# Performance work log

Hardware: AMD Instinct MI355X
Metric: run time of the kernel (lower is better)

The kernel has to match this reference:

```python
import jax, jax.numpy as jnp
import numpy as np

B, S, D = 4, 1024, 2048
NH, HD = 16, 128  # nhead, head_dim
SCALE = HD ** -0.5


def setup_inputs() -> dict:
    key = jax.random.key(0)
    ks = jax.random.split(key, 7)
    query = jax.random.normal(ks[0], (B, S, D), dtype=jnp.float32)
    key_t = jax.random.normal(ks[1], (B, S, D), dtype=jnp.float32)
    value = jax.random.normal(ks[2], (B, S, D), dtype=jnp.float32)
    # qkv_proj: Linear(D, 3D) with bias; out_proj: Linear(D, D) with bias
    Wqkv = jax.random.normal(ks[3], (3 * D, D), dtype=jnp.float32) * (D ** -0.5)
    bqkv = jnp.zeros((3 * D,), dtype=jnp.float32)
    Wout = jax.random.normal(ks[4], (D, D), dtype=jnp.float32) * (D ** -0.5)
    bout = jnp.zeros((D,), dtype=jnp.float32)
    return {"query": query, "key": key_t, "value": value,
            "Wqkv": Wqkv, "bqkv": bqkv, "Wout": Wout, "bout": bout}


def reference(query, key, value, Wqkv, bqkv, Wout, bout):
    # NOTE: module ignores `key`/`value` args; qkv comes from query alone.
    b, s, d = query.shape
    qkv = query @ Wqkv.T + bqkv                       # (B,S,3D)
    q, k, v = jnp.split(qkv, 3, axis=-1)
    q = q.reshape(b, s, NH, HD).transpose(0, 2, 1, 3) * SCALE  # (B,H,S,hd)
    k = k.reshape(b, s, NH, HD).transpose(0, 2, 1, 3)          # (B,H,S,hd)
    # faithful replication of the module's odd v permutation:
    v = v.reshape(b, s, HD, NH).transpose(0, 2, 1, 3)          # (B,hd,S,H)
    v = v.reshape(b, s, NH * HD).reshape(b, s, NH, HD).transpose(0, 2, 1, 3)  # (B,H,S,hd)
    scores = jnp.einsum('bhqd,bhkd->bhqk', q, k)               # (B,H,S,S)
    causal = jnp.triu(jnp.ones((s, s), dtype=bool), k=1)
    scores = jnp.where(causal, -jnp.inf, scores)
    attn = jax.nn.softmax(scores.astype(jnp.float32), axis=-1).astype(query.dtype)
    out = jnp.einsum('bhqk,bhkd->bhqd', attn, v)               # (B,H,S,hd)
    out = out.transpose(0, 2, 1, 3).reshape(b, s, d)
    return out @ Wout.T + bout
```

## Files before the change

kernel.cpp:

```cpp
#include <hip/hip_runtime.h>
#include <hip/hip_bf16.h>
#include <stdint.h>

typedef __bf16 bf16x8 __attribute__((ext_vector_type(8)));
typedef float  floatx4 __attribute__((ext_vector_type(4)));

#define NEG_BIG (-1e30f)

#define GLD16(g, l) __builtin_amdgcn_global_load_lds(                         \
    (__attribute__((address_space(1))) void*)(g),                             \
    (__attribute__((address_space(3))) void*)(l), 16, 0, 0)

__device__ __forceinline__ void cvt16(const float* __restrict__ s,
                                      __hip_bfloat16* __restrict__ d) {
    float4 f[4];
#pragma unroll
    for (int i = 0; i < 4; i++) f[i] = ((const float4*)s)[i];
    union { __hip_bfloat16 h[16]; uint4 u[2]; } o;
#pragma unroll
    for (int i = 0; i < 4; i++) {
        o.h[4 * i + 0] = __float2bfloat16(f[i].x);
        o.h[4 * i + 1] = __float2bfloat16(f[i].y);
        o.h[4 * i + 2] = __float2bfloat16(f[i].z);
        o.h[4 * i + 3] = __float2bfloat16(f[i].w);
    }
    ((uint4*)d)[0] = o.u[0];
    ((uint4*)d)[1] = o.u[1];
}

__global__ __launch_bounds__(256)
void cvt3_f32_bf16(const float* __restrict__ a, size_t na8,
                   const float* __restrict__ b, size_t nb8,
                   const float* __restrict__ c, size_t nc8,
                   __hip_bfloat16* __restrict__ da,
                   __hip_bfloat16* __restrict__ db,
                   __hip_bfloat16* __restrict__ dc)
{
    const size_t total  = na8 + nb8 + nc8;
    const size_t stride = (size_t)gridDim.x * blockDim.x;
    for (size_t idx = (size_t)blockIdx.x * blockDim.x + threadIdx.x;
         idx < total; idx += stride) {
        const float* s; __hip_bfloat16* d; size_t o;
        if (idx < na8)            { s = a; d = da; o = idx; }
        else if (idx < na8 + nb8) { s = b; d = db; o = idx - na8; }
        else                      { s = c; d = dc; o = idx - na8 - nb8; }
        const float4 f0 = ((const float4*)s)[o * 2 + 0];
        const float4 f1 = ((const float4*)s)[o * 2 + 1];
        union { __hip_bfloat16 h[8]; uint4 u; } z;
        z.h[0] = __float2bfloat16(f0.x); z.h[1] = __float2bfloat16(f0.y);
        z.h[2] = __float2bfloat16(f0.z); z.h[3] = __float2bfloat16(f0.w);
        z.h[4] = __float2bfloat16(f1.x); z.h[5] = __float2bfloat16(f1.y);
        z.h[6] = __float2bfloat16(f1.z); z.h[7] = __float2bfloat16(f1.w);
        ((uint4*)d)[o] = z.u;
    }
}

__global__ __launch_bounds__(256, 2)
void gemm2b_nt_bias(const __hip_bfloat16* __restrict__ A,
                    const __hip_bfloat16* __restrict__ B,
                    const float* __restrict__ bias,
                    __hip_bfloat16* __restrict__ C,
                    int M, int N, int K, int lda, int ldb)
{
    __shared__ __align__(16) __hip_bfloat16 Asm[2][128 * 64];
    __shared__ __align__(16) __hip_bfloat16 Bsm[2][192 * 64];

    const int flat = blockIdx.x;
    const int c    = flat & 7;
    const int i_   = flat >> 3;
    const int by = (c & 1) * 16 + (i_ & 15);
    const int bx = (c >> 1) * 8 + (i_ >> 4);
    const int m0 = by * 128, n0 = bx * 192;

    const int t    = threadIdx.x;
    const int wave = t >> 6, lane = t & 63;
    const int quad = lane >> 4, l16 = lane & 15;
    const int wr   = wave >> 1, wc = wave & 1;
    const int NT   = K >> 6;

    const int l8 = lane >> 3;
    const int g_ = (lane & 7) ^ l8;
    auto stageA = [&](int tk, int j, int buf) {
        GLD16(A + (size_t)(m0 + j * 32 + wave * 8 + l8) * lda + tk * 64 + g_ * 8,
              &Asm[buf][0] + (j * 32 + wave * 8) * 64);
    };
    auto stageB = [&](int tk, int j, int buf) {
        GLD16(B + (size_t)(n0 + j * 32 + wave * 8 + l8) * ldb + tk * 64 + g_ * 8,
              &Bsm[buf][0] + (j * 32 + wave * 8) * 64);
    };

    const int g0 = (quad ^ (l16 & 7)) << 3;

    floatx4 acc[4][6];
    const floatx4 zero = {0.f, 0.f, 0.f, 0.f};
#pragma unroll
    for (int mi = 0; mi < 4; mi++)
#pragma unroll
        for (int ni = 0; ni < 6; ni++) acc[mi][ni] = zero;

#pragma unroll
    for (int j = 0; j < 4; j++) stageA(0, j, 0);
#pragma unroll
    for (int j = 0; j < 6; j++) stageB(0, j, 0);
    if (NT > 1) {
        stageA(1, 0, 1); stageA(1, 2, 1);
        stageB(1, 0, 1); stageB(1, 1, 1); stageB(1, 2, 1);
        asm volatile("s_waitcnt vmcnt(5)" ::: "memory");
    } else {
        asm volatile("s_waitcnt vmcnt(0)" ::: "memory");
    }
    __syncthreads();

    int cb = 0;
    for (int tk = 0; tk < NT; ++tk, cb ^= 1) {
        const __hip_bfloat16* Ab = &Asm[cb][0];
        const __hip_bfloat16* Bb = &Bsm[cb][0];
        const int nb = cb ^ 1;

        bf16x8 af[2][2], bfr[6][2];
#pragma unroll
        for (int i = 0; i < 2; i++)
#pragma unroll
            for (int ks = 0; ks < 2; ks++)
                af[i][ks] = *(const bf16x8*)(
                    Ab + (wr * 64 + i * 16 + l16) * 64 + (g0 ^ (ks ? 32 : 0)));
#pragma unroll
        for (int ni = 0; ni < 6; ni++)
#pragma unroll
            for (int ks = 0; ks < 2; ks++)
                bfr[ni][ks] = *(const bf16x8*)(
                    Bb + (wc * 96 + ni * 16 + l16) * 64 + (g0 ^ (ks ? 32 : 0)));
        if (tk + 1 < NT) {
            stageA(tk + 1, 1, nb); stageA(tk + 1, 3, nb);
            stageB(tk + 1, 3, nb); stageB(tk + 1, 4, nb); stageB(tk + 1, 5, nb);
        }
        __builtin_amdgcn_s_barrier();
        asm volatile("s_waitcnt lgkmcnt(0)" ::: "memory");
        __builtin_amdgcn_s_setprio(1);
#pragma unroll
        for (int ks = 0; ks < 2; ks++)
#pragma unroll
            for (int i = 0; i < 2; i++)
#pragma unroll
                for (int ni = 0; ni < 6; ni++)
                    acc[i][ni] = __builtin_amdgcn_mfma_f32_16x16x32_bf16(
                        af[i][ks], bfr[ni][ks], acc[i][ni], 0, 0, 0);
        __builtin_amdgcn_s_setprio(0);
        __builtin_amdgcn_s_barrier();

#pragma unroll
        for (int i = 0; i < 2; i++)
#pragma unroll
            for (int ks = 0; ks < 2; ks++)
                af[i][ks] = *(const bf16x8*)(
                    Ab + (wr * 64 + (2 + i) * 16 + l16) * 64 + (g0 ^ (ks ? 32 : 0)));
        if (tk + 2 < NT) {
            stageA(tk + 2, 0, cb); stageA(tk + 2, 2, cb);
            stageB(tk + 2, 0, cb); stageB(tk + 2, 1, cb); stageB(tk + 2, 2, cb);
        }
        __builtin_amdgcn_s_barrier();
        asm volatile("s_waitcnt lgkmcnt(0)" ::: "memory");
        __builtin_amdgcn_s_setprio(1);
#pragma unroll
        for (int ks = 0; ks < 2; ks++)
#pragma unroll
            for (int i = 0; i < 2; i++)
#pragma unroll
                for (int ni = 0; ni < 6; ni++)
                    acc[2 + i][ni] = __builtin_amdgcn_mfma_f32_16x16x32_bf16(
                        af[i][ks], bfr[ni][ks], acc[2 + i][ni], 0, 0, 0);
        __builtin_amdgcn_s_setprio(0);
        if (tk + 2 < NT)
            asm volatile("s_waitcnt vmcnt(5)" ::: "memory");
        else if (tk + 1 < NT)
            asm volatile("s_waitcnt vmcnt(0)" ::: "memory");
        __builtin_amdgcn_s_barrier();
    }

#pragma unroll
    for (int mi = 0; mi < 4; mi++) {
        const int row = m0 + wr * 64 + mi * 16 + quad * 4;
#pragma unroll
        for (int ni = 0; ni < 6; ni++) {
            const int col = n0 + wc * 96 + ni * 16 + l16;
            const float bv = bias[col];
#pragma unroll
            for (int r = 0; r < 4; r++)
                C[(size_t)(row + r) * N + col] =
                    __float2bfloat16(acc[mi][ni][r] + bv);
        }
    }
}

template <bool OUT_F32>
__global__ __launch_bounds__(512, 2)
void gemm8p_nt_bias(const __hip_bfloat16* __restrict__ A,
                    const __hip_bfloat16* __restrict__ B,
                    const float* __restrict__ bias, void* __restrict__ Cv,
                    int M, int N, int K, int lda, int ldb, int nby)
{
    __shared__ __align__(16) __hip_bfloat16 Asm[2][128 * 64];
    __shared__ __align__(16) __hip_bfloat16 Bsm[2][256 * 64];

    const int nwg = gridDim.x, cpx = nwg >> 3;
    const int flat = blockIdx.x;
    const int swz  = (flat & 7) * cpx + (flat >> 3);
    const int by = swz % nby, bx = swz / nby;
    const int m0 = by * 128, n0 = bx * 256;

    const int t    = threadIdx.x;
    const int wave = t >> 6, lane = t & 63;
    const int quad = lane >> 4, l16 = lane & 15;
    const int wr   = wave >> 2, wc = wave & 3;
    const int NT   = K >> 6;

    const int l8 = lane >> 3;
    const int g_ = (lane & 7) ^ l8;
    const int aRowBase = (wave >> 2) * 64 + (wave & 3) * 8;
    const int bRowBase = wave * 8;

    auto stageA = [&](int tk, int j, int buf) {
        GLD16(A + (size_t)(m0 + aRowBase + j * 32 + l8) * lda + tk * 64 + g_ * 8,
              &Asm[buf][0] + (aRowBase + j * 32) * 64);
    };
    auto stageB = [&](int tk, int j, int buf) {
        GLD16(B + (size_t)(n0 + bRowBase + j * 64 + l8) * ldb + tk * 64 + g_ * 8,
              &Bsm[buf][0] + (bRowBase + j * 64) * 64);
    };

    const int g0 = (quad ^ (l16 & 7)) << 3;

    floatx4 acc[4][4];
    const floatx4 zero = {0.f, 0.f, 0.f, 0.f};
#pragma unroll
    for (int mi = 0; mi < 4; mi++)
#pragma unroll
        for (int ni = 0; ni < 4; ni++) acc[mi][ni] = zero;

    stageA(0, 0, 0); stageA(0, 1, 0);
    stageB(0, 0, 0); stageB(0, 1, 0); stageB(0, 2, 0); stageB(0, 3, 0);
    if (NT > 1) {
        stageA(1, 0, 1); stageB(1, 0, 1); stageB(1, 1, 1);
        asm volatile("s_waitcnt vmcnt(3)" ::: "memory");
    } else {
        asm volatile("s_waitcnt vmcnt(0)" ::: "memory");
    }
    __syncthreads();

    int cb = 0;
    for (int tk = 0; tk < NT; ++tk, cb ^= 1) {
        const __hip_bfloat16* Ab = &Asm[cb][0];
        const __hip_bfloat16* Bb = &Bsm[cb][0];
        const int nb = cb ^ 1;

        bf16x8 af[2][2], bfr[4][2];
#pragma unroll
        for (int i = 0; i < 2; i++)
#pragma unroll
            for (int ks = 0; ks < 2; ks++)
                af[i][ks] = *(const bf16x8*)(
                    Ab + (wr * 64 + i * 16 + l16) * 64 + (g0 ^ (ks ? 32 : 0)));
#pragma unroll
        for (int ni = 0; ni < 4; ni++)
#pragma unroll
            for (int ks = 0; ks < 2; ks++)
                bfr[ni][ks] = *(const bf16x8*)(
                    Bb + (wc * 64 + ni * 16 + l16) * 64 + (g0 ^ (ks ? 32 : 0)));
        if (tk + 1 < NT) {
            stageA(tk + 1, 1, nb); stageB(tk + 1, 2, nb); stageB(tk + 1, 3, nb);
        }
        __builtin_amdgcn_s_barrier();
        asm volatile("s_waitcnt lgkmcnt(0)" ::: "memory");
        __builtin_amdgcn_s_setprio(1);
#pragma unroll
        for (int ks = 0; ks < 2; ks++)
#pragma unroll
            for (int i = 0; i < 2; i++)
#pragma unroll
                for (int ni = 0; ni < 4; ni++)
                    acc[i][ni] = __builtin_amdgcn_mfma_f32_16x16x32_bf16(
                        af[i][ks], bfr[ni][ks], acc[i][ni], 0, 0, 0);
        __builtin_amdgcn_s_setprio(0);
        __builtin_amdgcn_s_barrier();

#pragma unroll
        for (int i = 0; i < 2; i++)
#pragma unroll
            for (int ks = 0; ks < 2; ks++)
                af[i][ks] = *(const bf16x8*)(
                    Ab + (wr * 64 + (2 + i) * 16 + l16) * 64 + (g0 ^ (ks ? 32 : 0)));
        if (tk + 2 < NT) {
            stageA(tk + 2, 0, cb); stageB(tk + 2, 0, cb); stageB(tk + 2, 1, cb);
        }
        __builtin_amdgcn_s_barrier();
        asm volatile("s_waitcnt lgkmcnt(0)" ::: "memory");
        __builtin_amdgcn_s_setprio(1);
#pragma unroll
        for (int ks = 0; ks < 2; ks++)
#pragma unroll
            for (int i = 0; i < 2; i++)
#pragma unroll
                for (int ni = 0; ni < 4; ni++)
                    acc[2 + i][ni] = __builtin_amdgcn_mfma_f32_16x16x32_bf16(
                        af[i][ks], bfr[ni][ks], acc[2 + i][ni], 0, 0, 0);
        __builtin_amdgcn_s_setprio(0);
        if (tk + 2 < NT)
            asm volatile("s_waitcnt vmcnt(3)" ::: "memory");
        else if (tk + 1 < NT)
            asm volatile("s_waitcnt vmcnt(0)" ::: "memory");
        __builtin_amdgcn_s_barrier();
    }

#pragma unroll
    for (int mi = 0; mi < 4; mi++) {
        const int row = m0 + wr * 64 + mi * 16 + quad * 4;
#pragma unroll
        for (int ni = 0; ni < 4; ni++) {
            const int col = n0 + wc * 64 + ni * 16 + l16;
            const float bv = bias[col];
#pragma unroll
            for (int r = 0; r < 4; r++) {
                const float v = acc[mi][ni][r] + bv;
                if (OUT_F32)
                    ((float*)Cv)[(size_t)(row + r) * N + col] = v;
                else
                    ((__hip_bfloat16*)Cv)[(size_t)(row + r) * N + col] =
                        __float2bfloat16(v);
            }
        }
    }
}

template <bool A_F32, bool B_F32, bool OUT_F32>
__global__ __launch_bounds__(256, 2)
void gemm_nt_bias(const void* __restrict__ Av, const void* __restrict__ Bv,
                  const float* __restrict__ bias, void* __restrict__ Cv,
                  int M, int N, int K, int lda, int ldb)
{
    __shared__ __align__(16) __hip_bfloat16 Asm[128 * 32];
    __shared__ __align__(16) __hip_bfloat16 Bsm[128 * 32];
    const int m0   = blockIdx.y * 128;
    const int n0   = blockIdx.x * 128;
    const int t    = threadIdx.x;
    const int wave = t >> 6, lane = t & 63;
    const int quad = lane >> 4, l16 = lane & 15;
    const int wr   = wave >> 1, wc = wave & 1;

    floatx4 zero = {0.f, 0.f, 0.f, 0.f};
    floatx4 acc[4][4];
    for (int i = 0; i < 4; i++)
        for (int j = 0; j < 4; j++) acc[i][j] = zero;

    for (int k0 = 0; k0 < K; k0 += 32) {
        if (A_F32) {
            const float* A = (const float*)Av;
            const int row = t >> 1, half = t & 1;
            cvt16(A + (size_t)(m0 + row) * lda + k0 + half * 16,
                  Asm + row * 32 + half * 16);
        } else {
            const __hip_bfloat16* A = (const __hip_bfloat16*)Av;
            for (int j = 0; j < 2; ++j) {
                const int chunk = (wave * 2 + j) * 64 + lane;
                const int row   = chunk >> 2;
                const int kc    = chunk & 3;
                GLD16(A + (size_t)(m0 + row) * lda + k0 + kc * 8,
                      Asm + (wave * 2 + j) * 512);
            }
        }
        if (B_F32) {
            const float* B = (const float*)Bv;
            const int row = t >> 1, half = t & 1;
            cvt16(B + (size_t)(n0 + row) * ldb + k0 + half * 16,
                  Bsm + row * 32 + half * 16);
        } else {
            const __hip_bfloat16* B = (const __hip_bfloat16*)Bv;
            for (int j = 0; j < 2; ++j) {
                const int chunk = (wave * 2 + j) * 64 + lane;
                const int row   = chunk >> 2;
                const int kc    = chunk & 3;
                GLD16(B + (size_t)(n0 + row) * ldb + k0 + kc * 8,
                      Bsm + (wave * 2 + j) * 512);
            }
        }
        __syncthreads();

        bf16x8 af[4], bf[4];
        for (int i = 0; i < 4; i++) {
            af[i] = *(const bf16x8*)(Asm + (wr * 64 + i * 16 + l16) * 32 + quad * 8);
            bf[i] = *(const bf16x8*)(Bsm + (wc * 64 + i * 16 + l16) * 32 + quad * 8);
        }
        for (int mi = 0; mi < 4; mi++)
            for (int ni = 0; ni < 4; ni++)
                acc[mi][ni] = __builtin_amdgcn_mfma_f32_16x16x32_bf16(
                    af[mi], bf[ni], acc[mi][ni], 0, 0, 0);
        __syncthreads();
    }

    for (int mi = 0; mi < 4; mi++) {
        const int row = m0 + wr * 64 + mi * 16 + quad * 4;
        for (int ni = 0; ni < 4; ni++) {
            const int col = n0 + wc * 64 + ni * 16 + l16;
            const float bv = bias[col];
            for (int r = 0; r < 4; r++) {
                const float v = acc[mi][ni][r] + bv;
                if (OUT_F32)
                    ((float*)Cv)[(size_t)(row + r) * N + col] = v;
                else
                    ((__hip_bfloat16*)Cv)[(size_t)(row + r) * N + col] =
                        __float2bfloat16(v);
            }
        }
    }
}

__global__ __launch_bounds__(256)
void permute_v(const __hip_bfloat16* __restrict__ QKV,
               __hip_bfloat16* __restrict__ Vpt)
{
    __shared__ __align__(16) __hip_bfloat16 S[64 * 64];
    const int blk = blockIdx.x;
    const int sb = blk & 31, h = (blk >> 5) & 15, b = blk >> 9;
    const int t = threadIdx.x;

    for (int j = 0; j < 2; j++) {
        const int chunk = j * 256 + t;
        const int lrow  = chunk >> 3;
        const int lcol  = (chunk & 7) * 8;
        const int r8 = lrow >> 3, jj = lrow & 7;
        const int srow = r8 * 128 + h * 8 + jj;
        const int scol = sb * 64 + lcol;
        *(uint4*)(S + chunk * 8) =
            *(const uint4*)(QKV + ((size_t)(b * 1024) + srow) * 6144 + 4096 + scol);
    }
    __syncthreads();

    const size_t obase = (((size_t)(b * 16 + h)) * 32 + sb) * 4096;
    for (int i = 0; i < 16; i++) {
        const int lin = t + 256 * i;
        const int hd = lin >> 5, ss = lin & 31;
        Vpt[obase + lin] =
            S[((ss & 7) * 8 + (hd >> 4)) * 64 + (ss >> 3) * 16 + (hd & 15)];
    }
}

__global__ __launch_bounds__(256, 2)
void flash_attn(const __hip_bfloat16* __restrict__ QKV,
                const __hip_bfloat16* __restrict__ Vpt,
                __hip_bfloat16* __restrict__ O)
{
    __shared__ __align__(16) __hip_bfloat16 Kt[2][64 * 128];
    __shared__ __align__(16) __hip_bfloat16 Vt[2][2 * 128 * 32];
    __shared__ __align__(16) __hip_bfloat16 Pl[64 * 64];

    const int bid  = blockIdx.x;
    const int pair = bid >> 6;
    const int g    = bid & 63;
    const int b    = g >> 4, h = g & 15;
    const int t    = threadIdx.x;
    const int wave = t >> 6, lane = t & 63;
    const int quad = lane >> 4, l16 = lane & 15;
    const float scale = 0.08838834764831845f;

    const int    rowb  = b * 1024;
    const size_t vbase = (((size_t)(b * 16 + h)) * 32) * 4096;
    const floatx4 zero = {0.f, 0.f, 0.f, 0.f};

    auto stageK = [&](int tk, int bufi) {
        const int kv0 = tk * 64;
        __hip_bfloat16* dst = &Kt[bufi][0];
#pragma unroll
        for (int j = 0; j < 4; j++) {
            const int c0 = (wave * 4 + j) * 64 + lane;
            const int r  = c0 >> 4;
            const int gg = (c0 & 15) ^ (r & 7);
            GLD16(QKV + ((size_t)(rowb + kv0 + r)) * 6144 + 2048 + h * 128 + gg * 8,
                  dst + (wave * 4 + j) * 512);
        }
    };
    auto stageV = [&](int tk, int bufi) {
        const __hip_bfloat16* src = Vpt + vbase + (size_t)(tk * 2) * 4096;
        __hip_bfloat16* dst = &Vt[bufi][0];
#pragma unroll
        for (int j = 0; j < 4; j++) {
            const int c0   = (wave * 4 + j) * 64 + lane;
            const int half = c0 >> 9, w = c0 & 511;
            const int r    = w >> 2;
            const int gg   = (w & 3) ^ (r & 3);
            GLD16(src + half * 4096 + r * 32 + gg * 8,
                  dst + (wave * 4 + j) * 512);
        }
    };

    for (int ph = 0; ph < 2; ++ph) {
        const int qb = ph ? (15 - pair) * 64 : pair * 64;
        const int nt = ph ? 16 - pair       : pair + 1;

        bf16x8 qf[4];
        {
            const size_t rb = ((size_t)(rowb + qb + wave * 16 + l16)) * 6144 + h * 128;
#pragma unroll
            for (int kc = 0; kc < 4; kc++)
                qf[kc] = *(const bf16x8*)(QKV + rb + kc * 32 + quad * 8);
        }

        float m_i[4], l_i[4];
        floatx4 oacc[8];
#pragma unroll
        for (int r = 0; r < 4; r++) { m_i[r] = NEG_BIG; l_i[r] = 0.f; }
#pragma unroll
        for (int ni = 0; ni < 8; ni++) oacc[ni] = zero;

        stageK(0, 0); stageV(0, 0);

        for (int tk = 0; tk < nt; ++tk) {
            const int cur = tk & 1;
            if (tk + 1 < nt) {
                stageK(tk + 1, cur ^ 1); stageV(tk + 1, cur ^ 1);
                asm volatile("s_waitcnt vmcnt(8)" ::: "memory");
            } else {
                asm volatile("s_waitcnt vmcnt(0)" ::: "memory");
            }
            __builtin_amdgcn_s_barrier();
            asm volatile("" ::: "memory");

            const __hip_bfloat16* Kb = &Kt[cur][0];
            const __hip_bfloat16* Vb = &Vt[cur][0];
            const int kv0 = tk * 64;

            floatx4 sc[4];
#pragma unroll
            for (int cbk = 0; cbk < 4; cbk++) {
                floatx4 s = zero;
                const int r  = cbk * 16 + l16;
                const int sw = r & 7;
#pragma unroll
                for (int kc = 0; kc < 4; kc++) {
                    bf16x8 kf = *(const bf16x8*)(
                        Kb + r * 128 + (((kc * 4 + quad) ^ sw) << 3));
                    s = __builtin_amdgcn_mfma_f32_16x16x32_bf16(qf[kc], kf, s, 0, 0, 0);
                }
                sc[cbk] = s;
            }

            const int qrow = qb + wave * 16 + quad * 4;
            if (tk == nt - 1) {
#pragma unroll
                for (int rr = 0; rr < 4; rr++)
#pragma unroll
                    for (int cbk = 0; cbk < 4; cbk++) {
                        const int col = kv0 + cbk * 16 + l16;
                        const float v = sc[cbk][rr] * scale;
                        sc[cbk][rr] = (col > qrow + rr) ? NEG_BIG : v;
                    }
            } else {
#pragma unroll
                for (int rr = 0; rr < 4; rr++)
#pragma unroll
                    for (int cbk = 0; cbk < 4; cbk++) sc[cbk][rr] *= scale;
            }
            float mx[4];
#pragma unroll
            for (int rr = 0; rr < 4; rr++)
                mx[rr] = fmaxf(fmaxf(sc[0][rr], sc[1][rr]),
                               fmaxf(sc[2][rr], sc[3][rr]));
#pragma unroll
            for (int off = 1; off < 16; off <<= 1)
#pragma unroll
                for (int rr = 0; rr < 4; rr++)
                    mx[rr] = fmaxf(mx[rr], __shfl_xor(mx[rr], off));

            float alpha[4], rsum[4];
#pragma unroll
            for (int rr = 0; rr < 4; rr++) {
                const float mnew = fmaxf(m_i[rr], mx[rr]);
                alpha[rr] = __expf(m_i[rr] - mnew);
                m_i[rr] = mnew;
                float acc = 0.f;
#pragma unroll
                for (int cbk = 0; cbk < 4; cbk++) {
                    const float pv = __expf(sc[cbk][rr] - mnew);
                    sc[cbk][rr] = pv;
                    acc += pv;
                }
                rsum[rr] = acc;
            }
#pragma unroll
            for (int off = 1; off < 16; off <<= 1)
#pragma unroll
                for (int rr = 0; rr < 4; rr++)
                    rsum[rr] += __shfl_xor(rsum[rr], off);
#pragma unroll
            for (int rr = 0; rr < 4; rr++)
                l_i[rr] = l_i[rr] * alpha[rr] + rsum[rr];
#pragma unroll
            for (int ni = 0; ni < 8; ni++)
#pragma unroll
                for (int rr = 0; rr < 4; rr++) oacc[ni][rr] *= alpha[rr];

#pragma unroll
            for (int cbk = 0; cbk < 4; cbk++)
#pragma unroll
                for (int rr = 0; rr < 4; rr++) {
                    const int row = wave * 16 + quad * 4 + rr;
                    const int col = cbk * 16 + l16;
                    Pl[row * 64 + ((((col >> 3) ^ (row & 7)) << 3) | (col & 7))] =
                        __float2bfloat16(sc[cbk][rr]);
                }
            asm volatile("s_waitcnt lgkmcnt(0)" ::: "memory");

            const int prow = wave * 16 + l16;
            bf16x8 pf[2];
#pragma unroll
            for (int kc = 0; kc < 2; kc++)
                pf[kc] = *(const bf16x8*)(
                    Pl + prow * 64 + (((kc * 4 + quad) ^ (prow & 7)) << 3));
#pragma unroll
            for (int ni = 0; ni < 8; ni++) {
                const int vr = ni * 16 + l16;
#pragma unroll
                for (int kc = 0; kc < 2; kc++) {
                    bf16x8 vf = *(const bf16x8*)(
                        Vb + kc * 4096 + vr * 32 + (((quad ^ (vr & 3))) << 3));
                    oacc[ni] = __builtin_amdgcn_mfma_f32_16x16x32_bf16(
                        pf[kc], vf, oacc[ni], 0, 0, 0);
                }
            }

            asm volatile("" ::: "memory");
            __builtin_amdgcn_s_barrier();
            asm volatile("" ::: "memory");
        }

        float inv[4];
#pragma unroll
        for (int rr = 0; rr < 4; rr++) inv[rr] = 1.0f / l_i[rr];
#pragma unroll
        for (int ni = 0; ni < 8; ni++)
#pragma unroll
            for (int rr = 0; rr < 4; rr++) {
                const int row = qb + wave * 16 + quad * 4 + rr;
                O[((size_t)rowb + row) * 6144 + 4096 + h * 128 + ni * 16 + l16] =
                    __float2bfloat16(oacc[ni][rr] * inv[rr]);
            }
    }
}

extern "C" void kernel_launch(void* const* d_in, const int* in_sizes, int n_in,
                              void* d_out, int out_size, void* d_ws, size_t ws_size,
                              hipStream_t stream) {
    const float* query = (const float*)d_in[0];
    const float* Wqkv = (const float*)d_in[3];
    const float* bqkv = (const float*)d_in[4];
    const float* Wout = (const float*)d_in[5];
    const float* bout = (const float*)d_in[6];
    float* out = (float*)d_out;

    const size_t MB = 1048576;
    char* ws = (char*)d_ws;
    __hip_bfloat16* QKV = (__hip_bfloat16*)ws;
    __hip_bfloat16* Vpt = (__hip_bfloat16*)(ws + 48 * MB);
    __hip_bfloat16* Att = QKV + 4096;

    dim3 blk(256);

    if (ws_size >= 113 * MB) {
        __hip_bfloat16* Qbf     = (__hip_bfloat16*)(ws + 64 * MB);
        __hip_bfloat16* Wqkv_bf = (__hip_bfloat16*)(ws + 80 * MB);
        __hip_bfloat16* Wout_bf = (__hip_bfloat16*)(ws + 104 * MB);

        cvt3_f32_bf16<<<dim3(2048), blk, 0, stream>>>(
            query, (size_t)4096 * 2048 / 8,
            Wqkv,  (size_t)6144 * 2048 / 8,
            Wout,  (size_t)2048 * 2048 / 8,
            Qbf, Wqkv_bf, Wout_bf);
        gemm2b_nt_bias<<<dim3(1024), dim3(256), 0, stream>>>(
            Qbf, Wqkv_bf, bqkv, QKV, 4096, 6144, 2048, 2048, 2048);
        permute_v<<<dim3(2048), blk, 0, stream>>>(QKV, Vpt);
        flash_attn<<<dim3(512), blk, 0, stream>>>(QKV, Vpt, QKV);
        gemm8p_nt_bias<true><<<dim3(256), dim3(512), 0, stream>>>(
            Att, Wout_bf, bout, out, 4096, 2048, 2048, 6144, 2048, 32);
    } else {
        gemm_nt_bias<true, true, false><<<dim3(48, 32), blk, 0, stream>>>(
            query, Wqkv, bqkv, QKV, 4096, 6144, 2048, 2048, 2048);
        permute_v<<<dim3(2048), blk, 0, stream>>>(QKV, Vpt);
        flash_attn<<<dim3(512), blk, 0, stream>>>(QKV, Vpt, QKV);
        gemm_nt_bias<false, true, true><<<dim3(16, 32), blk, 0, stream>>>(
            Att, Wout, bout, out, 4096, 2048, 2048, 6144, 2048);
    }
}
```

Measured before the change: 358.1 us.

## Use 128x128-tile out-proj GEMM and lazy softmax rescaling in flash attention

The 512-thread 128x256 output-projection GEMM is replaced by a 256-thread 128x128 tile kernel launched on 512 workgroups. It uses a new XCD-aware block swizzle and four A/B stage loads per tile. Flash attention now skips the running-max update and accumulator rescale unless some row's max grows by more than 8, a threshold chosen so exponentials stay bounded. The per-row sum reduction across lanes is deferred to the end of the loop. This trades exact per-step max tracking for fewer exp, shuffle and multiply operations, and raises GEMM occupancy at the cost of less operand reuse per tile.

```diff
diff --git a/kernel.cpp b/kernel.cpp
--- a/kernel.cpp
+++ b/kernel.cpp
@@ -192,40 +192,38 @@
     }
 }
 
-template <bool OUT_F32>
-__global__ __launch_bounds__(512, 2)
-void gemm8p_nt_bias(const __hip_bfloat16* __restrict__ A,
-                    const __hip_bfloat16* __restrict__ B,
-                    const float* __restrict__ bias, void* __restrict__ Cv,
-                    int M, int N, int K, int lda, int ldb, int nby)
+__global__ __launch_bounds__(256, 2)
+void gemm2b128_nt_bias(const __hip_bfloat16* __restrict__ A,
+                       const __hip_bfloat16* __restrict__ B,
+                       const float* __restrict__ bias,
+                       float* __restrict__ C,
+                       int M, int N, int K, int lda, int ldb)
 {
     __shared__ __align__(16) __hip_bfloat16 Asm[2][128 * 64];
-    __shared__ __align__(16) __hip_bfloat16 Bsm[2][256 * 64];
-
-    const int nwg = gridDim.x, cpx = nwg >> 3;
+    __shared__ __align__(16) __hip_bfloat16 Bsm[2][128 * 64];
+
     const int flat = blockIdx.x;
-    const int swz  = (flat & 7) * cpx + (flat >> 3);
-    const int by = swz % nby, bx = swz / nby;
-    const int m0 = by * 128, n0 = bx * 256;
+    const int c    = flat & 7;
+    const int i_   = flat >> 3;
+    const int by = (c & 3) * 8 + (i_ & 7);
+    const int bx = (c >> 2) * 8 + (i_ >> 3);
+    const int m0 = by * 128, n0 = bx * 128;
 
     const int t    = threadIdx.x;
     const int wave = t >> 6, lane = t & 63;
     const int quad = lane >> 4, l16 = lane & 15;
-    const int wr   = wave >> 2, wc = wave & 3;
+    const int wr   = wave >> 1, wc = wave & 1;
     const int NT   = K >> 6;
 
     const int l8 = lane >> 3;
     const int g_ = (lane & 7) ^ l8;
-    const int aRowBase = (wave >> 2) * 64 + (wave & 3) * 8;
-    const int bRowBase = wave * 8;
-
     auto stageA = [&](int tk, int j, int buf) {
-        GLD16(A + (size_t)(m0 + aRowBase + j * 32 + l8) * lda + tk * 64 + g_ * 8,
-              &Asm[buf][0] + (aRowBase + j * 32) * 64);
+        GLD16(A + (size_t)(m0 + j * 32 + wave * 8 + l8) * lda + tk * 64 + g_ * 8,
+              &Asm[buf][0] + (j * 32 + wave * 8) * 64);
     };
     auto stageB = [&](int tk, int j, int buf) {
-        GLD16(B + (size_t)(n0 + bRowBase + j * 64 + l8) * ldb + tk * 64 + g_ * 8,
-              &Bsm[buf][0] + (bRowBase + j * 64) * 64);
+        GLD16(B + (size_t)(n0 + j * 32 + wave * 8 + l8) * ldb + tk * 64 + g_ * 8,
+              &Bsm[buf][0] + (j * 32 + wave * 8) * 64);
     };
 
     const int g0 = (quad ^ (l16 & 7)) << 3;
@@ -237,11 +235,13 @@
 #pragma unroll
         for (int ni = 0; ni < 4; ni++) acc[mi][ni] = zero;
 
-    stageA(0, 0, 0); stageA(0, 1, 0);
-    stageB(0, 0, 0); stageB(0, 1, 0); stageB(0, 2, 0); stageB(0, 3, 0);
+#pragma unroll
+    for (int j = 0; j < 4; j++) stageA(0, j, 0);
+#pragma unroll
+    for (int j = 0; j < 4; j++) stageB(0, j, 0);
     if (NT > 1) {
-        stageA(1, 0, 1); stageB(1, 0, 1); stageB(1, 1, 1);
-        asm volatile("s_waitcnt vmcnt(3)" ::: "memory");
+        stageA(1, 0, 1); stageA(1, 2, 1); stageB(1, 0, 1); stageB(1, 1, 1);
+        asm volatile("s_waitcnt vmcnt(4)" ::: "memory");
     } else {
         asm volatile("s_waitcnt vmcnt(0)" ::: "memory");
     }
@@ -267,7 +267,8 @@
                 bfr[ni][ks] = *(const bf16x8*)(
                     Bb + (wc * 64 + ni * 16 + l16) * 64 + (g0 ^ (ks ? 32 : 0)));
         if (tk + 1 < NT) {
-            stageA(tk + 1, 1, nb); stageB(tk + 1, 2, nb); stageB(tk + 1, 3, nb);
+            stageA(tk + 1, 1, nb); stageA(tk + 1, 3, nb);
+            stageB(tk + 1, 2, nb); stageB(tk + 1, 3, nb);
         }
         __builtin_amdgcn_s_barrier();
         asm volatile("s_waitcnt lgkmcnt(0)" ::: "memory");
@@ -290,7 +291,8 @@
                 af[i][ks] = *(const bf16x8*)(
                     Ab + (wr * 64 + (2 + i) * 16 + l16) * 64 + (g0 ^ (ks ? 32 : 0)));
         if (tk + 2 < NT) {
-            stageA(tk + 2, 0, cb); stageB(tk + 2, 0, cb); stageB(tk + 2, 1, cb);
+            stageA(tk + 2, 0, cb); stageA(tk + 2, 2, cb);
+            stageB(tk + 2, 0, cb); stageB(tk + 2, 1, cb);
         }
         __builtin_amdgcn_s_barrier();
         asm volatile("s_waitcnt lgkmcnt(0)" ::: "memory");
@@ -305,7 +307,7 @@
                         af[i][ks], bfr[ni][ks], acc[2 + i][ni], 0, 0, 0);
         __builtin_amdgcn_s_setprio(0);
         if (tk + 2 < NT)
-            asm volatile("s_waitcnt vmcnt(3)" ::: "memory");
+            asm volatile("s_waitcnt vmcnt(4)" ::: "memory");
         else if (tk + 1 < NT)
             asm volatile("s_waitcnt vmcnt(0)" ::: "memory");
         __builtin_amdgcn_s_barrier();
@@ -319,14 +321,8 @@
             const int col = n0 + wc * 64 + ni * 16 + l16;
             const float bv = bias[col];
 #pragma unroll
-            for (int r = 0; r < 4; r++) {
-                const float v = acc[mi][ni][r] + bv;
-                if (OUT_F32)
-                    ((float*)Cv)[(size_t)(row + r) * N + col] = v;
-                else
-                    ((__hip_bfloat16*)Cv)[(size_t)(row + r) * N + col] =
-                        __float2bfloat16(v);
-            }
+            for (int r = 0; r < 4; r++)
+                C[(size_t)(row + r) * N + col] = acc[mi][ni][r] + bv;
         }
     }
 }
@@ -569,33 +565,40 @@
                 for (int rr = 0; rr < 4; rr++)
                     mx[rr] = fmaxf(mx[rr], __shfl_xor(mx[rr], off));
 
-            float alpha[4], rsum[4];
-#pragma unroll
-            for (int rr = 0; rr < 4; rr++) {
-                const float mnew = fmaxf(m_i[rr], mx[rr]);
-                alpha[rr] = __expf(m_i[rr] - mnew);
-                m_i[rr] = mnew;
-                float acc = 0.f;
-#pragma unroll
-                for (int cbk = 0; cbk < 4; cbk++) {
-                    const float pv = __expf(sc[cbk][rr] - mnew);
-                    sc[cbk][rr] = pv;
-                    acc += pv;
+            bool grow = false;
+#pragma unroll
+            for (int rr = 0; rr < 4; rr++)
+                grow = grow || (mx[rr] > m_i[rr] + 8.0f);
+            if (__any((int)grow)) {
+#pragma unroll
+                for (int rr = 0; rr < 4; rr++) {
+                    const float mnew  = fmaxf(m_i[rr], mx[rr]);
+                    const float alpha = __expf(m_i[rr] - mnew);
+                    m_i[rr] = mnew;
+                    float lsum = 0.f;
+#pragma unroll
+                    for (int cbk = 0; cbk < 4; cbk++) {
+                        const float pv = __expf(sc[cbk][rr] - mnew);
+                        sc[cbk][rr] = pv;
+                        lsum += pv;
+                    }
+                    l_i[rr] = l_i[rr] * alpha + lsum;
+#pragma unroll
+                    for (int ni = 0; ni < 8; ni++) oacc[ni][rr] *= alpha;
                 }
-                rsum[rr] = acc;
-            }
-#pragma unroll
-            for (int off = 1; off < 16; off <<= 1)
-#pragma unroll
-                for (int rr = 0; rr < 4; rr++)
-                    rsum[rr] += __shfl_xor(rsum[rr], off);
-#pragma unroll
-            for (int rr = 0; rr < 4; rr++)
-                l_i[rr] = l_i[rr] * alpha[rr] + rsum[rr];
-#pragma unroll
-            for (int ni = 0; ni < 8; ni++)
-#pragma unroll
-                for (int rr = 0; rr < 4; rr++) oacc[ni][rr] *= alpha[rr];
+            } else {
+#pragma unroll
+                for (int rr = 0; rr < 4; rr++) {
+                    float lsum = 0.f;
+#pragma unroll
+                    for (int cbk = 0; cbk < 4; cbk++) {
+                        const float pv = __expf(sc[cbk][rr] - m_i[rr]);
+                        sc[cbk][rr] = pv;
+                        lsum += pv;
+                    }
+                    l_i[rr] += lsum;
+                }
+            }
 
 #pragma unroll
             for (int cbk = 0; cbk < 4; cbk++)
@@ -631,6 +634,11 @@
             asm volatile("" ::: "memory");
         }
 
+#pragma unroll
+        for (int off = 1; off < 16; off <<= 1)
+#pragma unroll
+            for (int rr = 0; rr < 4; rr++)
+                l_i[rr] += __shfl_xor(l_i[rr], off);
         float inv[4];
 #pragma unroll
         for (int rr = 0; rr < 4; rr++) inv[rr] = 1.0f / l_i[rr];
@@ -677,8 +685,8 @@
             Qbf, Wqkv_bf, bqkv, QKV, 4096, 6144, 2048, 2048, 2048);
         permute_v<<<dim3(2048), blk, 0, stream>>>(QKV, Vpt);
         flash_attn<<<dim3(512), blk, 0, stream>>>(QKV, Vpt, QKV);
-        gemm8p_nt_bias<true><<<dim3(256), dim3(512), 0, stream>>>(
-            Att, Wout_bf, bout, out, 4096, 2048, 2048, 6144, 2048, 32);
+        gemm2b128_nt_bias<<<dim3(512), dim3(256), 0, stream>>>(
+            Att, Wout_bf, bout, out, 4096, 2048, 2048, 6144, 2048);
     } else {
         gemm_nt_bias<true, true, false><<<dim3(48, 32), blk, 0, stream>>>(
             query, Wqkv, bqkv, QKV, 4096, 6144, 2048, 2048, 2048);
```

Measured after the change: 354.9 us. No clear change (-0.9%).
